# Performance work log

Measured on AMD Instinct MI355X. Metric: run time of the kernel, lower is better.

The kernel has to match this reference:

```python
import jax, jax.numpy as jnp
import numpy as np

B, T = 2, 512
E, NH, HD, V, P, L, KER, BLOCK = 768, 12, 64, 256, 4, 4, 16, 512
SCALE = HD ** -0.5


def _ln(x, g, b, eps=1e-5):
    m = jnp.mean(x, -1, keepdims=True)
    v = jnp.mean((x - m) ** 2, -1, keepdims=True)
    return (x - m) * jax.lax.rsqrt(v + eps) * g + b


def _rope_tables(n):
    inv = 1.0 / (10000.0 ** (jnp.arange(0, HD, 2, dtype=jnp.float32) / HD))
    f = jnp.arange(n, dtype=jnp.float32)[:, None] * inv[None, :]
    return jnp.cos(f), jnp.sin(f)


def _rope(x, cos, sin):
    # rotate over last two dims (positions, HD); split-half RoPE as in source
    h = x.shape[-1] // 2
    x1, x2 = x[..., :h], x[..., h:]
    return jnp.concatenate([x1 * cos - x2 * sin, x1 * sin + x2 * cos], axis=-1)


def _patch_attn(x, qkv_w, S):
    # x: [B,T,E]; sliding-window patch attention, step=1
    Bb, Tt, _ = x.shape
    q, k, v = jnp.split(x @ qkv_w, 3, axis=-1)
    heads = lambda t: t.reshape(Bb, Tt, NH, HD).transpose(0, 2, 1, 3)  # [B,NH,T,HD]
    q, k, v = heads(q), heads(k), heads(v)
    cos, sin = _rope_tables(Tt)
    q = _rope(q, cos, sin)
    k = _rope(k, cos, sin)
    # prefix: full causal attention over first S tokens
    sc = jnp.einsum('bnqh,bnkh->bnqk', q[:, :, :S], k[:, :, :S]) * SCALE
    mask = jnp.tril(jnp.ones((S, S), dtype=bool))
    sc = jnp.where(mask, sc, jnp.float32(-jnp.inf))
    out = jnp.einsum('bnqk,bnkh->bnqh', jax.nn.softmax(sc, axis=-1), v[:, :, :S])
    if Tt > S:
        # query t (t>=S) attends keys [t-S+1, t] (mask_sliding is all-ones for step=1)
        idx = jnp.arange(Tt - S)[:, None] + 1 + jnp.arange(S)[None, :]  # [T-S,S]
        kw = k[:, :, idx]  # [B,NH,T-S,S,HD]
        vw = v[:, :, idx]
        qs = q[:, :, S:]   # [B,NH,T-S,HD]
        sw = jnp.einsum('bnth,bntsh->bnts', qs, kw) * SCALE
        ow = jnp.einsum('bnts,bntsh->bnth', jax.nn.softmax(sw, axis=-1), vw)
        out = jnp.concatenate([out, ow], axis=2)
    return out.transpose(0, 2, 1, 3).reshape(Bb, Tt, NH * HD)


def _sa_block(x, ln0g, ln0b, ln1g, ln1b, qkv_w, proj_w, proj_b, w1, b1, w2, b2):
    # x: [B,T,P,V]; full (unmasked) attention over the P prediction slots
    Bb, Tt, Pp, _ = x.shape
    h = _ln(x, ln0g, ln0b)
    q, k, v = jnp.split(h @ qkv_w, 3, axis=-1)
    heads = lambda t: t.reshape(Bb, Tt, Pp, NH, HD).transpose(0, 1, 3, 2, 4)  # [B,T,NH,P,HD]
    q, k, v = heads(q), heads(k), heads(v)
    cos, sin = _rope_tables(Pp)
    q = _rope(q, cos, sin)
    k = _rope(k, cos, sin)
    sc = jnp.einsum('btnph,btnqh->btnpq', q, k) * SCALE
    o = jnp.einsum('btnpq,btnqh->btnph', jax.nn.softmax(sc, axis=-1), v)
    o = o.transpose(0, 1, 3, 2, 4).reshape(Bb, Tt, Pp, NH * HD)
    x = x + (o @ proj_w + proj_b)
    h2 = _ln(x, ln1g, ln1b)
    ff = jax.nn.gelu(h2 @ w1 + b1, approximate=False) @ w2 + b2
    return x + ff


def _forward(tokens, emb, blk_ln0_g, blk_ln0_b, blk_ln1_g, blk_ln1_b, blk_qkv_w,
             blk_ff_w1, blk_ff_b1, blk_ff_w2, blk_ff_b2, fin_ln_g, fin_ln_b,
             head_w, head_b, sa_ln0_g, sa_ln0_b, sa_ln1_g, sa_ln1_b, sa_qkv_w,
             sa_proj_w, sa_proj_b, sa_ff_w1, sa_ff_b1, sa_ff_w2, sa_ff_b2):
    x0 = emb[tokens]  # [B,T,E]
    x = x0
    for i in range(L):
        S = min(KER * 2 ** i, BLOCK)
        h = _ln(x, blk_ln0_g[i], blk_ln0_b[i])
        x = x + _patch_attn(h, blk_qkv_w[i], S)
        h2 = _ln(x, blk_ln1_g[i], blk_ln1_b[i])
        x = x + (jax.nn.gelu(h2 @ blk_ff_w1[i] + blk_ff_b1[i], approximate=False)
                 @ blk_ff_w2[i] + blk_ff_b2[i])
    x = x0 + x  # Golu: x = token_embedding(x); x = x + blocks(x)
    x = _ln(x, fin_ln_g, fin_ln_b)
    logits = (x @ head_w + head_b).reshape(B, T, P, V)
    logits = _sa_block(logits, sa_ln0_g, sa_ln0_b, sa_ln1_g, sa_ln1_b, sa_qkv_w,
                       sa_proj_w, sa_proj_b, sa_ff_w1, sa_ff_b1, sa_ff_w2, sa_ff_b2)
    return logits[:, :, 0, :]  # [B,T,V] (y is None path)


def setup_inputs() -> dict:
    key = jax.random.key(0)
    ks = jax.random.split(key, 12)
    w = lambda k, sh: jax.random.normal(k, sh, dtype=jnp.float32) * 0.02
    return {
        'tokens': jax.random.randint(ks[0], (B, T), 0, V),
        'emb': w(ks[1], (V, E)),
        'blk_ln0_g': jnp.ones((L, E), jnp.float32),
        'blk_ln0_b': jnp.zeros((L, E), jnp.float32),
        'blk_ln1_g': jnp.ones((L, E), jnp.float32),
        'blk_ln1_b': jnp.zeros((L, E), jnp.float32),
        'blk_qkv_w': w(ks[2], (L, E, 3 * E)),
        'blk_ff_w1': w(ks[3], (L, E, 4 * E)),
        'blk_ff_b1': jnp.zeros((L, 4 * E), jnp.float32),
        'blk_ff_w2': w(ks[4], (L, 4 * E, E)),
        'blk_ff_b2': jnp.zeros((L, E), jnp.float32),
        'fin_ln_g': jnp.ones((E,), jnp.float32),
        'fin_ln_b': jnp.zeros((E,), jnp.float32),
        'head_w': w(ks[5], (E, V * P)),
        'head_b': jnp.zeros((V * P,), jnp.float32),
        'sa_ln0_g': jnp.ones((V,), jnp.float32),
        'sa_ln0_b': jnp.zeros((V,), jnp.float32),
        'sa_ln1_g': jnp.ones((V,), jnp.float32),
        'sa_ln1_b': jnp.zeros((V,), jnp.float32),
        'sa_qkv_w': w(ks[6], (V, 3 * E)),
        'sa_proj_w': w(ks[7], (E, V)),
        'sa_proj_b': jnp.zeros((V,), jnp.float32),
        'sa_ff_w1': w(ks[8], (V, 4 * V)),
        'sa_ff_b1': jnp.zeros((4 * V,), jnp.float32),
        'sa_ff_w2': w(ks[9], (4 * V, V)),
        'sa_ff_b2': jnp.zeros((V,), jnp.float32),
    }


def reference(tokens, emb, blk_ln0_g, blk_ln0_b, blk_ln1_g, blk_ln1_b, blk_qkv_w,
              blk_ff_w1, blk_ff_b1, blk_ff_w2, blk_ff_b2, fin_ln_g, fin_ln_b,
              head_w, head_b, sa_ln0_g, sa_ln0_b, sa_ln1_g, sa_ln1_b, sa_qkv_w,
              sa_proj_w, sa_proj_b, sa_ff_w1, sa_ff_b1, sa_ff_w2, sa_ff_b2):
    return _forward(tokens, emb, blk_ln0_g, blk_ln0_b, blk_ln1_g, blk_ln1_b,
                    blk_qkv_w, blk_ff_w1, blk_ff_b1, blk_ff_w2, blk_ff_b2,
                    fin_ln_g, fin_ln_b, head_w, head_b, sa_ln0_g, sa_ln0_b,
                    sa_ln1_g, sa_ln1_b, sa_qkv_w, sa_proj_w, sa_proj_b,
                    sa_ff_w1, sa_ff_b1, sa_ff_w2, sa_ff_b2)
```

## Files before the change

kernel.cpp:

```cpp
#include <hip/hip_runtime.h>
#include <hip/hip_bf16.h>
#include <cstdint>
#include <cstddef>

#define BB    2
#define TSEQ  512
#define EDIM  768
#define NHEAD 12
#define HDIM  64
#define VDIM  256
#define PDIM  4
#define NROW  (BB*TSEQ)
#define NROW2 (BB*TSEQ*PDIM)

typedef __attribute__((ext_vector_type(8))) short short8;
typedef __attribute__((ext_vector_type(4))) short short4v;
typedef __attribute__((ext_vector_type(4))) float floatx4;

__device__ __forceinline__ float gelu_f(float v){
    return 0.5f * v * (1.0f + erff(v * 0.70710678118654752f));
}
__device__ __forceinline__ float b2f(short s){
    unsigned u = ((unsigned)(unsigned short)s) << 16;
    float f; __builtin_memcpy(&f, &u, 4); return f;
}
__device__ __forceinline__ short f2bs(float v){
    __hip_bfloat16 h = __float2bfloat16(v);
    short s; __builtin_memcpy(&s, &h, 2); return s;
}
__device__ __forceinline__ void gload16(const void* g, void* l){
    __builtin_amdgcn_global_load_lds((const __attribute__((address_space(1))) void*)g,
                                     (__attribute__((address_space(3))) void*)l, 16, 0, 0);
}

#define WAITN(n) asm volatile("s_waitcnt vmcnt(" #n ")" ::: "memory")
#define WAIT_STAGE(rem, full, half)                         \
    do{ if((rem) >= 2)      WAITN(full);                    \
        else if((rem) == 1) WAITN(half);                    \
        else                WAITN(0);                       \
        asm volatile("s_barrier" ::: "memory"); }while(0)

struct WD2 { const float* in; __hip_bfloat16* out; int K; int N; int nt; };
struct WDs { WD2 d[17]; };

__global__ __launch_bounds__(256) void wconv_all(WDs a)
{
    int id = blockIdx.x;
    int i = 0;
    while(i < 16 && id >= a.d[i].nt){ id -= a.d[i].nt; i++; }
    WD2 w = a.d[i];
    const int tx = w.N / 128;
    const int n0 = (id % tx) * 128, k0 = (id / tx) * 128;
    __shared__ short t[128*128];
    {
        const int c4 = (threadIdx.x & 31) * 4;
        const int r0 = threadIdx.x >> 5;
        #pragma unroll
        for(int half = 0; half < 2; half++){
            float4 v[8];
            #pragma unroll
            for(int it = 0; it < 8; it++){
                int r = r0 + it*8 + half*64;
                v[it] = *(const float4*)(w.in + (size_t)(k0 + r) * w.N + n0 + c4);
            }
            #pragma unroll
            for(int it = 0; it < 8; it++){
                int r = r0 + it*8 + half*64;
                int nswz = c4 ^ (((r >> 3) & 15) << 2);
                short4v o;
                o[0] = f2bs(v[it].x); o[1] = f2bs(v[it].y);
                o[2] = f2bs(v[it].z); o[3] = f2bs(v[it].w);
                *(short4v*)&t[r*128 + nswz] = o;
            }
        }
    }
    __syncthreads();
    {
        const int k8 = (threadIdx.x & 15) * 8;
        const int nr = threadIdx.x >> 4;
        const int swz = (k8 >> 3) << 2;
        #pragma unroll
        for(int pass = 0; pass < 8; pass++){
            int n = nr + pass*16;
            int nswz = n ^ swz;
            short8 o;
            #pragma unroll
            for(int j = 0; j < 8; j++) o[j] = t[(k8 + j)*128 + nswz];
            *(short8*)((short*)w.out + (size_t)(n0 + n) * w.K + k0 + k8) = o;
        }
    }
}

template<int ACT, int RESID, int OUTBF16, int ROPESA>
__global__ __launch_bounds__(256) void gemm128(
    const short* __restrict__ A, const short* __restrict__ Bt,
    const float* __restrict__ bias, const float* __restrict__ resid,
    void* __restrict__ Cout, const float* __restrict__ rc, const float* __restrict__ rs,
    int M, int N, int K)
{
    alignas(16) __shared__ short As[4*128*32];
    alignas(16) __shared__ short Bs[4*128*32];
    const int tid  = threadIdx.x;
    const int lane = tid & 63;
    const int wave = tid >> 6;
    const int bm = blockIdx.y * 128, bn = blockIdx.x * 128;
    const int wm = (wave >> 1) * 64, wn = (wave & 1) * 64;
    const int quad = lane >> 4, l16 = lane & 15;

    floatx4 acc[4][4];
    #pragma unroll
    for(int i = 0; i < 4; i++)
        #pragma unroll
        for(int j = 0; j < 4; j++)
            acc[i][j] = floatx4{0.f, 0.f, 0.f, 0.f};

    const int r  = tid >> 2;
    const int c8 = (tid & 3) * 8;
    const int ldsoff = (tid & 192) * 16;

    auto issue = [&](int k0, int cur){
        char* ab = (char*)As + cur*8192 + ldsoff;
        char* bb = (char*)Bs + cur*8192 + ldsoff;
        gload16(A  + (size_t)(bm + r     ) * K + k0 + c8, ab);
        gload16(A  + (size_t)(bm + r + 64) * K + k0 + c8, ab + 4096);
        gload16(Bt + (size_t)(bn + r     ) * K + k0 + c8, bb);
        gload16(Bt + (size_t)(bn + r + 64) * K + k0 + c8, bb + 4096);
    };

    const int niter = K >> 5;
    issue(0, 0); issue(32, 1); issue(64, 2);
    for(int it = 0; it < niter; it++){
        WAIT_STAGE(niter - 1 - it, 8, 4);
        if(it + 3 < niter) issue((it + 3) << 5, (it + 3) & 3);
        const short* Ab = As + (it & 3) * 4096;
        const short* Bb = Bs + (it & 3) * 4096;
        short8 af[4], bfr[4];
        #pragma unroll
        for(int i = 0; i < 4; i++){
            af[i]  = *(const short8*)&Ab[(wm + i*16 + l16)*32 + quad*8];
            bfr[i] = *(const short8*)&Bb[(wn + i*16 + l16)*32 + quad*8];
        }
        #pragma unroll
        for(int i = 0; i < 4; i++)
            #pragma unroll
            for(int j = 0; j < 4; j++)
                acc[i][j] = __builtin_amdgcn_mfma_f32_16x16x32_bf16(af[i], bfr[j], acc[i][j], 0, 0, 0);
    }

    float* Cf = (float*)Cout;
    __hip_bfloat16* Cb = (__hip_bfloat16*)Cout;

    if(ROPESA){
        const int hb = bn + wn;
        const int region = hb / 768;
        #pragma unroll
        for(int i = 0; i < 4; i++){
            #pragma unroll
            for(int rr = 0; rr < 4; rr++){
                int row = bm + wm + i*16 + quad*4 + rr;
                float a0 = acc[i][0][rr], a1 = acc[i][1][rr];
                float a2 = acc[i][2][rr], a3 = acc[i][3][rr];
                size_t rowb = (size_t)row * N + hb;
                if(region == 2){
                    Cb[rowb + l16]      = __float2bfloat16(a0);
                    Cb[rowb + 16 + l16] = __float2bfloat16(a1);
                    Cb[rowb + 32 + l16] = __float2bfloat16(a2);
                    Cb[rowb + 48 + l16] = __float2bfloat16(a3);
                }else{
                    int p = row & 3;
                    float c0 = rc[p*32 + l16],      s0 = rs[p*32 + l16];
                    float c1 = rc[p*32 + 16 + l16], s1 = rs[p*32 + 16 + l16];
                    Cb[rowb + l16]      = __float2bfloat16(a0*c0 - a2*s0);
                    Cb[rowb + 16 + l16] = __float2bfloat16(a1*c1 - a3*s1);
                    Cb[rowb + 32 + l16] = __float2bfloat16(a0*s0 + a2*c0);
                    Cb[rowb + 48 + l16] = __float2bfloat16(a1*s1 + a3*c1);
                }
            }
        }
        return;
    }

    #pragma unroll
    for(int i = 0; i < 4; i++){
        int row0 = bm + wm + i*16 + quad*4;
        #pragma unroll
        for(int j = 0; j < 4; j++){
            int col = bn + wn + j*16 + l16;
            float bv = bias ? bias[col] : 0.f;
            #pragma unroll
            for(int rr = 0; rr < 4; rr++){
                float v = acc[i][j][rr] + bv;
                if(ACT) v = gelu_f(v);
                if(RESID) v += resid[(size_t)(row0 + rr) * N + col];
                if(OUTBF16) Cb[(size_t)(row0 + rr) * N + col] = __float2bfloat16(v);
                else        Cf[(size_t)(row0 + rr) * N + col] = v;
            }
        }
    }
}

template<int EPI>
__global__ __launch_bounds__(256) void gemm64x128(
    const short* __restrict__ A, const short* __restrict__ Bt,
    const float* __restrict__ bias, __hip_bfloat16* __restrict__ Cout,
    __hip_bfloat16* __restrict__ qrb, __hip_bfloat16* __restrict__ krb,
    __hip_bfloat16* __restrict__ vvb,
    const float* __restrict__ rc, const float* __restrict__ rs,
    int M, int N, int K)
{
    alignas(16) __shared__ short As[4*64*32];
    alignas(16) __shared__ short Bs[4*128*32];
    const int tid  = threadIdx.x;
    const int lane = tid & 63;
    const int wave = tid >> 6;
    const int bm = blockIdx.y * 64, bn = blockIdx.x * 128;
    const int wm = (wave >> 1) * 32, wn = (wave & 1) * 64;
    const int quad = lane >> 4, l16 = lane & 15;

    floatx4 acc[2][4];
    #pragma unroll
    for(int i = 0; i < 2; i++)
        #pragma unroll
        for(int j = 0; j < 4; j++)
            acc[i][j] = floatx4{0.f, 0.f, 0.f, 0.f};

    const int r  = tid >> 2;
    const int c8 = (tid & 3) * 8;
    const int ldsoff = (tid & 192) * 16;

    auto issue = [&](int k0, int cur){
        char* ab = (char*)As + cur*4096 + ldsoff;
        char* bb = (char*)Bs + cur*8192 + ldsoff;
        gload16(A  + (size_t)(bm + r     ) * K + k0 + c8, ab);
        gload16(Bt + (size_t)(bn + r     ) * K + k0 + c8, bb);
        gload16(Bt + (size_t)(bn + r + 64) * K + k0 + c8, bb + 4096);
    };

    const int niter = K >> 5;
    issue(0, 0); issue(32, 1); issue(64, 2);
    for(int it = 0; it < niter; it++){
        WAIT_STAGE(niter - 1 - it, 6, 3);
        if(it + 3 < niter) issue((it + 3) << 5, (it + 3) & 3);
        const short* Ab = As + (it & 3) * 2048;
        const short* Bb = Bs + (it & 3) * 4096;
        short8 af[2], bfr[4];
        #pragma unroll
        for(int i = 0; i < 2; i++)
            af[i]  = *(const short8*)&Ab[(wm + i*16 + l16)*32 + quad*8];
        #pragma unroll
        for(int j = 0; j < 4; j++)
            bfr[j] = *(const short8*)&Bb[(wn + j*16 + l16)*32 + quad*8];
        #pragma unroll
        for(int i = 0; i < 2; i++)
            #pragma unroll
            for(int j = 0; j < 4; j++)
                acc[i][j] = __builtin_amdgcn_mfma_f32_16x16x32_bf16(af[i], bfr[j], acc[i][j], 0, 0, 0);
    }

    if(EPI == 2){
        const int hb = bn + wn;
        const int region = hb / 768;
        const int h = (hb % 768) >> 6;
        #pragma unroll
        for(int i = 0; i < 2; i++){
            #pragma unroll
            for(int rr = 0; rr < 4; rr++){
                int row = bm + wm + i*16 + quad*4 + rr;
                int t = row & (TSEQ-1), b = row >> 9;
                float a0 = acc[i][0][rr], a1 = acc[i][1][rr];
                float a2 = acc[i][2][rr], a3 = acc[i][3][rr];
                size_t dbase = ((size_t)(b*NHEAD + h)*TSEQ + t)*HDIM;
                if(region == 2){
                    vvb[dbase + l16]      = __float2bfloat16(a0);
                    vvb[dbase + 16 + l16] = __float2bfloat16(a1);
                    vvb[dbase + 32 + l16] = __float2bfloat16(a2);
                    vvb[dbase + 48 + l16] = __float2bfloat16(a3);
                }else{
                    float c0 = rc[t*32 + l16],      s0 = rs[t*32 + l16];
                    float c1 = rc[t*32 + 16 + l16], s1 = rs[t*32 + 16 + l16];
                    __hip_bfloat16* dst = (region == 0) ? qrb : krb;
                    dst[dbase + l16]      = __float2bfloat16(a0*c0 - a2*s0);
                    dst[dbase + 16 + l16] = __float2bfloat16(a1*c1 - a3*s1);
                    dst[dbase + 32 + l16] = __float2bfloat16(a0*s0 + a2*c0);
                    dst[dbase + 48 + l16] = __float2bfloat16(a1*s1 + a3*c1);
                }
            }
        }
        return;
    }

    #pragma unroll
    for(int i = 0; i < 2; i++){
        int row0 = bm + wm + i*16 + quad*4;
        #pragma unroll
        for(int j = 0; j < 4; j++){
            int col = bn + wn + j*16 + l16;
            float bv = bias ? bias[col] : 0.f;
            #pragma unroll
            for(int rr = 0; rr < 4; rr++){
                float v = acc[i][j][rr] + bv;
                if(EPI == 1) v = gelu_f(v);
                Cout[(size_t)(row0 + rr) * N + col] = __float2bfloat16(v);
            }
        }
    }
}

template<int RESID, int OUTC>
__global__ __launch_bounds__(256) void gemm64t(
    const short* __restrict__ A, const short* __restrict__ Bt,
    const float* __restrict__ bias, const float* __restrict__ resid,
    float* __restrict__ Cf, float* __restrict__ outp, int M, int N, int K)
{
    alignas(16) __shared__ short As[4*64*32];
    alignas(16) __shared__ short Bs[4*64*32];
    const int tid  = threadIdx.x;
    const int lane = tid & 63;
    const int wave = tid >> 6;
    const int bm = blockIdx.y * 64, bn = blockIdx.x * 64;
    const int wm = (wave >> 1) * 32, wn = (wave & 1) * 32;
    const int quad = lane >> 4, l16 = lane & 15;

    floatx4 acc[2][2];
    #pragma unroll
    for(int i = 0; i < 2; i++)
        #pragma unroll
        for(int j = 0; j < 2; j++)
            acc[i][j] = floatx4{0.f, 0.f, 0.f, 0.f};

    const int r  = tid >> 2;
    const int c8 = (tid & 3) * 8;
    const int ldsoff = (tid & 192) * 16;

    auto issue = [&](int k0, int cur){
        char* ab = (char*)As + cur*4096 + ldsoff;
        char* bb = (char*)Bs + cur*4096 + ldsoff;
        gload16(A  + (size_t)(bm + r) * K + k0 + c8, ab);
        gload16(Bt + (size_t)(bn + r) * K + k0 + c8, bb);
    };

    const int niter = K >> 5;
    issue(0, 0); issue(32, 1); issue(64, 2);
    for(int it = 0; it < niter; it++){
        WAIT_STAGE(niter - 1 - it, 4, 2);
        if(it + 3 < niter) issue((it + 3) << 5, (it + 3) & 3);
        const short* Ab = As + (it & 3) * 2048;
        const short* Bb = Bs + (it & 3) * 2048;
        short8 af[2], bfr[2];
        #pragma unroll
        for(int i = 0; i < 2; i++){
            af[i]  = *(const short8*)&Ab[(wm + i*16 + l16)*32 + quad*8];
            bfr[i] = *(const short8*)&Bb[(wn + i*16 + l16)*32 + quad*8];
        }
        #pragma unroll
        for(int i = 0; i < 2; i++)
            #pragma unroll
            for(int j = 0; j < 2; j++)
                acc[i][j] = __builtin_amdgcn_mfma_f32_16x16x32_bf16(af[i], bfr[j], acc[i][j], 0, 0, 0);
    }

    #pragma unroll
    for(int i = 0; i < 2; i++){
        int row0 = bm + wm + i*16 + quad*4;
        #pragma unroll
        for(int j = 0; j < 2; j++){
            int col = bn + wn + j*16 + l16;
            float bv = bias ? bias[col] : 0.f;
            #pragma unroll
            for(int rr = 0; rr < 4; rr++){
                int row = row0 + rr;
                float v = acc[i][j][rr] + bv;
                if(RESID) v += resid[(size_t)row * N + col];
                Cf[(size_t)row * N + col] = v;
                if(OUTC && (row & 3) == 0)
                    outp[(size_t)(row >> 2) * N + col] = v;
            }
        }
    }
}

template<int D>
__global__ __launch_bounds__(256) void ln_wave(
    const float* __restrict__ in, const float* __restrict__ in2,
    const float* __restrict__ g, const float* __restrict__ bta,
    __hip_bfloat16* __restrict__ out)
{
    constexpr int NC = D / 256;
    const int row  = blockIdx.x * 4 + (threadIdx.x >> 6);
    const int lane = threadIdx.x & 63;
    const float* xr = in + (size_t)row * D;
    float4 v[NC];
    float sum = 0.f, sq = 0.f;
    #pragma unroll
    for(int j = 0; j < NC; j++){
        int d0 = (lane + 64*j) * 4;
        v[j] = *(const float4*)(xr + d0);
        if(in2){
            float4 u = *(const float4*)(in2 + (size_t)row * D + d0);
            v[j].x += u.x; v[j].y += u.y; v[j].z += u.z; v[j].w += u.w;
        }
        sum += v[j].x + v[j].y + v[j].z + v[j].w;
        sq  += v[j].x*v[j].x + v[j].y*v[j].y + v[j].z*v[j].z + v[j].w*v[j].w;
    }
    #pragma unroll
    for(int off = 32; off > 0; off >>= 1){
        sum += __shfl_xor(sum, off, 64);
        sq  += __shfl_xor(sq,  off, 64);
    }
    const float m    = sum / D;
    const float rstd = rsqrtf(fmaxf(sq / D - m*m, 0.f) + 1e-5f);
    #pragma unroll
    for(int j = 0; j < NC; j++){
        int d0 = (lane + 64*j) * 4;
        float4 gg = *(const float4*)(g + d0);
        float4 bb = *(const float4*)(bta + d0);
        short4v o;
        o[0] = f2bs((v[j].x - m) * rstd * gg.x + bb.x);
        o[1] = f2bs((v[j].y - m) * rstd * gg.y + bb.y);
        o[2] = f2bs((v[j].z - m) * rstd * gg.z + bb.z);
        o[3] = f2bs((v[j].w - m) * rstd * gg.w + bb.w);
        *(short4v*)((short*)out + (size_t)row * D + d0) = o;
    }
}

__global__ __launch_bounds__(192) void embed_kernel(
    const int* __restrict__ tokens, const float* __restrict__ emb,
    float* __restrict__ x0, float* __restrict__ x)
{
    const int row = blockIdx.x;
    const int tok = tokens[row];
    const float4* src = (const float4*)(emb + (size_t)tok * EDIM);
    float4* d0 = (float4*)(x0 + (size_t)row * EDIM);
    float4* d1 = (float4*)(x  + (size_t)row * EDIM);
    for(int i = threadIdx.x; i < EDIM/4; i += blockDim.x){
        float4 v = src[i]; d0[i] = v; d1[i] = v;
    }
}

__global__ __launch_bounds__(256) void rope_kernel(float* __restrict__ rc, float* __restrict__ rs)
{
    int i = blockIdx.x * 256 + threadIdx.x;
    int pos = i >> 5, d = i & 31;
    float inv = powf(10000.0f, -(float)(2*d) / 64.0f);
    float f = (float)pos * inv;
    rc[i] = cosf(f);
    rs[i] = sinf(f);
}

template<int S>
__global__ __launch_bounds__(256) void patch_attn16(
    const __hip_bfloat16* __restrict__ qr, const __hip_bfloat16* __restrict__ kr,
    const __hip_bfloat16* __restrict__ vv, float* __restrict__ x)
{
    constexpr int W = S + 15;
    alignas(16) __shared__ short Ks[W*64];
    alignas(16) __shared__ short Vs[W*64];
    __shared__ float qlds[16*64];
    __shared__ float pb[16*128];

    const int t0 = blockIdx.x * 16;
    const int h = blockIdx.y, b = blockIdx.z;
    const int tid = threadIdx.x;
    const int wv = tid >> 6, lane = tid & 63;
    const size_t headbase = ((size_t)(b*NHEAD + h)) * TSEQ;

    const int c = tid & 7;
    for(int r = tid >> 3; r < W; r += 32){
        int g = t0 - S + 1 + r;
        int gc = g < 0 ? 0 : g;
        int sc = (c ^ (r & 7)) * 8;
        *(short8*)&Ks[r*64 + sc] = *(const short8*)((const short*)kr + (headbase + gc)*64 + c*8);
        *(short8*)&Vs[r*64 + sc] = *(const short8*)((const short*)vv + (headbase + gc)*64 + c*8);
    }
    for(int i = tid; i < 16*64; i += 256)
        qlds[i] = __bfloat162float(qr[(headbase + t0 + (i >> 6))*64 + (i & 63)]);
    __syncthreads();

    #pragma unroll
    for(int qq = 0; qq < 4; qq++){
        const int ql = wv*4 + qq;
        const int t  = t0 + ql;
        const int r0 = (S >= 64) ? (ql + lane) : ((lane < S) ? (ql + lane) : 0);
        const int r1 = ql + lane + 64;
        float a0 = 0.f, a1 = 0.f;
        #pragma unroll
        for(int ch = 0; ch < 8; ch++){
            float4 qa = *(const float4*)&qlds[ql*64 + ch*8];
            float4 qb = *(const float4*)&qlds[ql*64 + ch*8 + 4];
            short8 k0 = *(const short8*)&Ks[r0*64 + ((ch ^ (r0 & 7))*8)];
            a0 += qa.x*b2f(k0[0]) + qa.y*b2f(k0[1]) + qa.z*b2f(k0[2]) + qa.w*b2f(k0[3])
                + qb.x*b2f(k0[4]) + qb.y*b2f(k0[5]) + qb.z*b2f(k0[6]) + qb.w*b2f(k0[7]);
            if(S == 128){
                short8 k1 = *(const short8*)&Ks[r1*64 + ((ch ^ (r1 & 7))*8)];
                a1 += qa.x*b2f(k1[0]) + qa.y*b2f(k1[1]) + qa.z*b2f(k1[2]) + qa.w*b2f(k1[3])
                    + qb.x*b2f(k1[4]) + qb.y*b2f(k1[5]) + qb.z*b2f(k1[6]) + qb.w*b2f(k1[7]);
            }
        }
        const int key0 = t - S + 1 + lane;
        const bool v0 = (lane < S) && (key0 >= 0);
        const bool v1 = (S == 128) && (key0 + 64 >= 0);
        float s0 = v0 ? a0 * 0.125f : -1e30f;
        float s1 = v1 ? a1 * 0.125f : -1e30f;
        float mx = fmaxf(s0, s1);
        #pragma unroll
        for(int off = 32; off > 0; off >>= 1) mx = fmaxf(mx, __shfl_xor(mx, off, 64));
        float p0 = v0 ? expf(s0 - mx) : 0.f;
        float p1 = v1 ? expf(s1 - mx) : 0.f;
        float sm = p0 + p1;
        #pragma unroll
        for(int off = 32; off > 0; off >>= 1) sm += __shfl_xor(sm, off, 64);
        const float inv = 1.f / sm;
        pb[ql*128 + lane] = p0 * inv;
        if(S == 128) pb[ql*128 + lane + 64] = p1 * inv;
    }

    const int d = lane;
    const int coff = d >> 3, dlo = d & 7;
    #pragma unroll
    for(int qq = 0; qq < 4; qq++){
        const int ql = wv*4 + qq;
        float o = 0.f;
        #pragma unroll 8
        for(int j = 0; j < S; j++){
            int r = ql + j;
            float p = pb[ql*128 + j];
            o += p * b2f(Vs[r*64 + ((coff ^ (r & 7))*8) + dlo]);
        }
        x[((size_t)(b*TSEQ) + t0 + ql) * EDIM + h*HDIM + d] += o;
    }
}

__global__ __launch_bounds__(256) void sa_attn(
    const __hip_bfloat16* __restrict__ qkv2, __hip_bfloat16* __restrict__ o)
{
    const int t = blockIdx.x, h = blockIdx.y, b = blockIdx.z;
    const int p = threadIdx.x >> 6, lane = threadIdx.x & 63;
    const int row0 = (b*TSEQ + t) * PDIM;
    const short* base = (const short*)qkv2 + (size_t)row0 * (3*EDIM);
    const int d = lane;
    float q = b2f(base[(size_t)p*(3*EDIM) + h*HDIM + d]);
    float sc[4];
    #pragma unroll
    for(int j = 0; j < 4; j++){
        float kj = b2f(base[(size_t)j*(3*EDIM) + EDIM + h*HDIM + d]);
        float v = q * kj;
        #pragma unroll
        for(int off = 32; off > 0; off >>= 1) v += __shfl_xor(v, off, 64);
        sc[j] = v * 0.125f;
    }
    float m = fmaxf(fmaxf(sc[0], sc[1]), fmaxf(sc[2], sc[3]));
    float e0 = expf(sc[0]-m), e1 = expf(sc[1]-m), e2 = expf(sc[2]-m), e3 = expf(sc[3]-m);
    float idn = 1.f / (e0 + e1 + e2 + e3);
    float ov = (e0 * b2f(base[0*(3*EDIM) + 2*EDIM + h*HDIM + d])
              + e1 * b2f(base[1*(3*EDIM) + 2*EDIM + h*HDIM + d])
              + e2 * b2f(base[2*(3*EDIM) + 2*EDIM + h*HDIM + d])
              + e3 * b2f(base[3*(3*EDIM) + 2*EDIM + h*HDIM + d])) * idn;
    o[(size_t)(row0 + p) * EDIM + h*HDIM + d] = __float2bfloat16(ov);
}

extern "C" void kernel_launch(void* const* d_in, const int* in_sizes, int n_in,
                              void* d_out, int out_size, void* d_ws, size_t ws_size,
                              hipStream_t stream)
{
    const int*   tokens    = (const int*)  d_in[0];
    const float* emb       = (const float*)d_in[1];
    const float* bl0g      = (const float*)d_in[2];
    const float* bl0b      = (const float*)d_in[3];
    const float* bl1g      = (const float*)d_in[4];
    const float* bl1b      = (const float*)d_in[5];
    const float* qkv_w     = (const float*)d_in[6];
    const float* ff_w1     = (const float*)d_in[7];
    const float* ff_b1     = (const float*)d_in[8];
    const float* ff_w2     = (const float*)d_in[9];
    const float* ff_b2     = (const float*)d_in[10];
    const float* fin_g     = (const float*)d_in[11];
    const float* fin_b     = (const float*)d_in[12];
    const float* head_w    = (const float*)d_in[13];
    const float* head_b    = (const float*)d_in[14];
    const float* sa_ln0_g  = (const float*)d_in[15];
    const float* sa_ln0_b  = (const float*)d_in[16];
    const float* sa_ln1_g  = (const float*)d_in[17];
    const float* sa_ln1_b  = (const float*)d_in[18];
    const float* sa_qkv_w  = (const float*)d_in[19];
    const float* sa_proj_w = (const float*)d_in[20];
    const float* sa_proj_b = (const float*)d_in[21];
    const float* sa_ff_w1  = (const float*)d_in[22];
    const float* sa_ff_b1  = (const float*)d_in[23];
    const float* sa_ff_w2  = (const float*)d_in[24];
    const float* sa_ff_b2  = (const float*)d_in[25];
    float* out = (float*)d_out;

    char* p = (char*)d_ws;
    auto alloc = [&](size_t bytes){ char* q = p; p += (bytes + 255) & ~(size_t)255; return q; };

    float* logits = (float*)alloc((size_t)NROW2*VDIM*4);
    float* ropec  = (float*)alloc(512*32*4);
    float* ropes  = (float*)alloc(512*32*4);
    __hip_bfloat16* wqkvT[4]; for(int i=0;i<4;i++) wqkvT[i] = (__hip_bfloat16*)alloc((size_t)768*2304*2);
    __hip_bfloat16* wff1T[4]; for(int i=0;i<4;i++) wff1T[i] = (__hip_bfloat16*)alloc((size_t)768*3072*2);
    __hip_bfloat16* wff2T[4]; for(int i=0;i<4;i++) wff2T[i] = (__hip_bfloat16*)alloc((size_t)3072*768*2);
    __hip_bfloat16* wheadT   = (__hip_bfloat16*)alloc((size_t)768*1024*2);
    __hip_bfloat16* wsaqkvT  = (__hip_bfloat16*)alloc((size_t)256*2304*2);
    __hip_bfloat16* wsaprojT = (__hip_bfloat16*)alloc((size_t)768*256*2);
    __hip_bfloat16* wsaff1T  = (__hip_bfloat16*)alloc((size_t)256*1024*2);
    __hip_bfloat16* wsaff2T  = (__hip_bfloat16*)alloc((size_t)1024*256*2);
    char* U = p;
    float* x0           = (float*)(U);
    float* x            = (float*)(U + 3145728);
    __hip_bfloat16* h   = (__hip_bfloat16*)(U + 6291456);
    __hip_bfloat16* ff1 = (__hip_bfloat16*)(U + 7864320);
    __hip_bfloat16* qrb = (__hip_bfloat16*)(U + 14155776);
    __hip_bfloat16* krb = (__hip_bfloat16*)(U + 15728640);
    __hip_bfloat16* vvb = (__hip_bfloat16*)(U + 17301504);
    __hip_bfloat16* h2    = (__hip_bfloat16*)(U);
    __hip_bfloat16* qkv2  = (__hip_bfloat16*)(U + 2097152);
    __hip_bfloat16* sa_o  = (__hip_bfloat16*)(U + 20971520);
    __hip_bfloat16* sa_f1 = (__hip_bfloat16*)(U + 27262976);

    embed_kernel<<<NROW, 192, 0, stream>>>(tokens, emb, x0, x);
    rope_kernel<<<64, 256, 0, stream>>>(ropec, ropes);
    {
        WDs wds; int tot = 0, n = 0;
        auto add = [&](const float* in, __hip_bfloat16* o2, int K, int N){
            wds.d[n++] = WD2{in, o2, K, N, (N/128)*(K/128)};
            tot += (N/128)*(K/128);
        };
        for(int i=0;i<4;i++){
            add(qkv_w + (size_t)i*768*2304, wqkvT[i], 768, 2304);
            add(ff_w1 + (size_t)i*768*3072, wff1T[i], 768, 3072);
            add(ff_w2 + (size_t)i*3072*768, wff2T[i], 3072, 768);
        }
        add(head_w,    wheadT,   768, 1024);
        add(sa_qkv_w,  wsaqkvT,  256, 2304);
        add(sa_proj_w, wsaprojT, 768, 256);
        add(sa_ff_w1,  wsaff1T,  256, 1024);
        add(sa_ff_w2,  wsaff2T, 1024, 256);
        wconv_all<<<tot, 256, 0, stream>>>(wds);
    }

    for(int i = 0; i < 4; i++){
        ln_wave<EDIM><<<NROW/4, 256, 0, stream>>>(x, nullptr, bl0g + i*EDIM, bl0b + i*EDIM, h);
        gemm64x128<2><<<dim3(18, 16), 256, 0, stream>>>(
            (const short*)h, (const short*)wqkvT[i], nullptr, nullptr,
            qrb, krb, vvb, ropec, ropes, NROW, 3*EDIM, EDIM);
        dim3 agrid(TSEQ/16, NHEAD, BB);
        if(i == 0)      patch_attn16<16><<<agrid, 256, 0, stream>>>(qrb, krb, vvb, x);
        else if(i == 1) patch_attn16<32><<<agrid, 256, 0, stream>>>(qrb, krb, vvb, x);
        else if(i == 2) patch_attn16<64><<<agrid, 256, 0, stream>>>(qrb, krb, vvb, x);
        else            patch_attn16<128><<<agrid, 256, 0, stream>>>(qrb, krb, vvb, x);
        ln_wave<EDIM><<<NROW/4, 256, 0, stream>>>(x, nullptr, bl1g + i*EDIM, bl1b + i*EDIM, h);
        gemm64x128<1><<<dim3(24, 16), 256, 0, stream>>>(
            (const short*)h, (const short*)wff1T[i], ff_b1 + (size_t)i*4*EDIM, ff1,
            nullptr, nullptr, nullptr, nullptr, nullptr, NROW, 4*EDIM, EDIM);
        gemm64t<1,0><<<dim3(12, 16), 256, 0, stream>>>(
            (const short*)ff1, (const short*)wff2T[i], ff_b2 + (size_t)i*EDIM, x, x, nullptr,
            NROW, EDIM, 4*EDIM);
    }

    ln_wave<EDIM><<<NROW/4, 256, 0, stream>>>(x, x0, fin_g, fin_b, h);
    gemm64t<0,0><<<dim3(16, 16), 256, 0, stream>>>(
        (const short*)h, (const short*)wheadT, head_b, nullptr, logits, nullptr,
        NROW, PDIM*VDIM, EDIM);

    ln_wave<VDIM><<<NROW2/4, 256, 0, stream>>>(logits, nullptr, sa_ln0_g, sa_ln0_b, h2);
    gemm128<0,0,1,1><<<dim3(18, 32), 256, 0, stream>>>(
        (const short*)h2, (const short*)wsaqkvT, nullptr, nullptr, qkv2,
        ropec, ropes, NROW2, 3*EDIM, VDIM);
    sa_attn<<<dim3(TSEQ, NHEAD, BB), 256, 0, stream>>>(qkv2, sa_o);
    gemm64t<1,0><<<dim3(4, 64), 256, 0, stream>>>(
        (const short*)sa_o, (const short*)wsaprojT, sa_proj_b, logits, logits, nullptr,
        NROW2, VDIM, EDIM);
    ln_wave<VDIM><<<NROW2/4, 256, 0, stream>>>(logits, nullptr, sa_ln1_g, sa_ln1_b, h2);
    gemm128<1,0,1,0><<<dim3(8, 32), 256, 0, stream>>>(
        (const short*)h2, (const short*)wsaff1T, sa_ff_b1, nullptr, sa_f1,
        nullptr, nullptr, NROW2, 4*VDIM, VDIM);
    gemm64t<1,1><<<dim3(4, 64), 256, 0, stream>>>(
        (const short*)sa_f1, (const short*)wsaff2T, sa_ff_b2, logits, logits, out,
        NROW2, VDIM, 4*VDIM);
}
```

Measured before the change: 698.8 us.

## Move QKV and FF1 GEMMs to 128x128 tiles, fuse embed/rope, loop heads in sa_attn

Drops the 64x128 GEMM kernel and runs the transformer-block QKV and FF1 GEMMs with the 128x128 gemm128 kernel, which gains a RoPE/head-scatter epilogue mode. Embedding and RoPE table generation are merged into one launch. sa_attn now loops over all 12 heads within a block instead of launching one block per head. Larger tiles give more operand reuse per block, but the grids shrink to 144 and 192 blocks, which may underfill the GPU's compute units. The sa_attn change does more serial work per block and launches 12x fewer blocks.

```diff
diff --git a/kernel.cpp b/kernel.cpp
--- a/kernel.cpp
+++ b/kernel.cpp
@@ -96,6 +96,8 @@
     const short* __restrict__ A, const short* __restrict__ Bt,
     const float* __restrict__ bias, const float* __restrict__ resid,
     void* __restrict__ Cout, const float* __restrict__ rc, const float* __restrict__ rs,
+    __hip_bfloat16* __restrict__ qrb, __hip_bfloat16* __restrict__ krb,
+    __hip_bfloat16* __restrict__ vvb,
     int M, int N, int K)
 {
     alignas(16) __shared__ short As[4*128*32];
@@ -150,7 +152,7 @@
     float* Cf = (float*)Cout;
     __hip_bfloat16* Cb = (__hip_bfloat16*)Cout;
 
-    if(ROPESA){
+    if(ROPESA == 1){
         const int hb = bn + wn;
         const int region = hb / 768;
         #pragma unroll
@@ -180,89 +182,12 @@
         return;
     }
 
-    #pragma unroll
-    for(int i = 0; i < 4; i++){
-        int row0 = bm + wm + i*16 + quad*4;
-        #pragma unroll
-        for(int j = 0; j < 4; j++){
-            int col = bn + wn + j*16 + l16;
-            float bv = bias ? bias[col] : 0.f;
-            #pragma unroll
-            for(int rr = 0; rr < 4; rr++){
-                float v = acc[i][j][rr] + bv;
-                if(ACT) v = gelu_f(v);
-                if(RESID) v += resid[(size_t)(row0 + rr) * N + col];
-                if(OUTBF16) Cb[(size_t)(row0 + rr) * N + col] = __float2bfloat16(v);
-                else        Cf[(size_t)(row0 + rr) * N + col] = v;
-            }
-        }
-    }
-}
-
-template<int EPI>
-__global__ __launch_bounds__(256) void gemm64x128(
-    const short* __restrict__ A, const short* __restrict__ Bt,
-    const float* __restrict__ bias, __hip_bfloat16* __restrict__ Cout,
-    __hip_bfloat16* __restrict__ qrb, __hip_bfloat16* __restrict__ krb,
-    __hip_bfloat16* __restrict__ vvb,
-    const float* __restrict__ rc, const float* __restrict__ rs,
-    int M, int N, int K)
-{
-    alignas(16) __shared__ short As[4*64*32];
-    alignas(16) __shared__ short Bs[4*128*32];
-    const int tid  = threadIdx.x;
-    const int lane = tid & 63;
-    const int wave = tid >> 6;
-    const int bm = blockIdx.y * 64, bn = blockIdx.x * 128;
-    const int wm = (wave >> 1) * 32, wn = (wave & 1) * 64;
-    const int quad = lane >> 4, l16 = lane & 15;
-
-    floatx4 acc[2][4];
-    #pragma unroll
-    for(int i = 0; i < 2; i++)
-        #pragma unroll
-        for(int j = 0; j < 4; j++)
-            acc[i][j] = floatx4{0.f, 0.f, 0.f, 0.f};
-
-    const int r  = tid >> 2;
-    const int c8 = (tid & 3) * 8;
-    const int ldsoff = (tid & 192) * 16;
-
-    auto issue = [&](int k0, int cur){
-        char* ab = (char*)As + cur*4096 + ldsoff;
-        char* bb = (char*)Bs + cur*8192 + ldsoff;
-        gload16(A  + (size_t)(bm + r     ) * K + k0 + c8, ab);
-        gload16(Bt + (size_t)(bn + r     ) * K + k0 + c8, bb);
-        gload16(Bt + (size_t)(bn + r + 64) * K + k0 + c8, bb + 4096);
-    };
-
-    const int niter = K >> 5;
-    issue(0, 0); issue(32, 1); issue(64, 2);
-    for(int it = 0; it < niter; it++){
-        WAIT_STAGE(niter - 1 - it, 6, 3);
-        if(it + 3 < niter) issue((it + 3) << 5, (it + 3) & 3);
-        const short* Ab = As + (it & 3) * 2048;
-        const short* Bb = Bs + (it & 3) * 4096;
-        short8 af[2], bfr[4];
-        #pragma unroll
-        for(int i = 0; i < 2; i++)
-            af[i]  = *(const short8*)&Ab[(wm + i*16 + l16)*32 + quad*8];
-        #pragma unroll
-        for(int j = 0; j < 4; j++)
-            bfr[j] = *(const short8*)&Bb[(wn + j*16 + l16)*32 + quad*8];
-        #pragma unroll
-        for(int i = 0; i < 2; i++)
-            #pragma unroll
-            for(int j = 0; j < 4; j++)
-                acc[i][j] = __builtin_amdgcn_mfma_f32_16x16x32_bf16(af[i], bfr[j], acc[i][j], 0, 0, 0);
-    }
-
-    if(EPI == 2){
+    if(ROPESA == 2){
         const int hb = bn + wn;
         const int region = hb / 768;
         const int h = (hb % 768) >> 6;
         #pragma unroll
-        for(int i = 0; i < 2; i++){
+        for(int i = 0; i < 4; i++){
             #pragma unroll
             for(int rr = 0; rr < 4; rr++){
                 int row = bm + wm + i*16 + quad*4 + rr;
@@ -290,7 +215,7 @@
     }
 
     #pragma unroll
-    for(int i = 0; i < 2; i++){
+    for(int i = 0; i < 4; i++){
         int row0 = bm + wm + i*16 + quad*4;
         #pragma unroll
         for(int j = 0; j < 4; j++){
@@ -299,8 +224,10 @@
             #pragma unroll
             for(int rr = 0; rr < 4; rr++){
                 float v = acc[i][j][rr] + bv;
-                if(EPI == 1) v = gelu_f(v);
-                Cout[(size_t)(row0 + rr) * N + col] = __float2bfloat16(v);
+                if(ACT) v = gelu_f(v);
+                if(RESID) v += resid[(size_t)(row0 + rr) * N + col];
+                if(OUTBF16) Cb[(size_t)(row0 + rr) * N + col] = __float2bfloat16(v);
+                else        Cf[(size_t)(row0 + rr) * N + col] = v;
             }
         }
     }
@@ -423,23 +350,23 @@
     }
 }
 
-__global__ __launch_bounds__(192) void embed_kernel(
+__global__ __launch_bounds__(256) void embed_rope(
     const int* __restrict__ tokens, const float* __restrict__ emb,
-    float* __restrict__ x0, float* __restrict__ x)
-{
-    const int row = blockIdx.x;
-    const int tok = tokens[row];
-    const float4* src = (const float4*)(emb + (size_t)tok * EDIM);
-    float4* d0 = (float4*)(x0 + (size_t)row * EDIM);
-    float4* d1 = (float4*)(x  + (size_t)row * EDIM);
-    for(int i = threadIdx.x; i < EDIM/4; i += blockDim.x){
-        float4 v = src[i]; d0[i] = v; d1[i] = v;
-    }
-}
-
-__global__ __launch_bounds__(256) void rope_kernel(float* __restrict__ rc, float* __restrict__ rs)
-{
-    int i = blockIdx.x * 256 + threadIdx.x;
+    float* __restrict__ x0, float* __restrict__ x,
+    float* __restrict__ rc, float* __restrict__ rs)
+{
+    const int blk = blockIdx.x;
+    if(blk < NROW){
+        const int tok = tokens[blk];
+        const float4* src = (const float4*)(emb + (size_t)tok * EDIM);
+        float4* d0 = (float4*)(x0 + (size_t)blk * EDIM);
+        float4* d1 = (float4*)(x  + (size_t)blk * EDIM);
+        if(threadIdx.x < EDIM/4){
+            float4 v = src[threadIdx.x]; d0[threadIdx.x] = v; d1[threadIdx.x] = v;
+        }
+        return;
+    }
+    int i = (blk - NROW) * 256 + threadIdx.x;
     int pos = i >> 5, d = i & 31;
     float inv = powf(10000.0f, -(float)(2*d) / 64.0f);
     float f = (float)pos * inv;
@@ -533,29 +460,31 @@
 __global__ __launch_bounds__(256) void sa_attn(
     const __hip_bfloat16* __restrict__ qkv2, __hip_bfloat16* __restrict__ o)
 {
-    const int t = blockIdx.x, h = blockIdx.y, b = blockIdx.z;
+    const int t = blockIdx.x, b = blockIdx.z;
     const int p = threadIdx.x >> 6, lane = threadIdx.x & 63;
     const int row0 = (b*TSEQ + t) * PDIM;
     const short* base = (const short*)qkv2 + (size_t)row0 * (3*EDIM);
     const int d = lane;
-    float q = b2f(base[(size_t)p*(3*EDIM) + h*HDIM + d]);
-    float sc[4];
-    #pragma unroll
-    for(int j = 0; j < 4; j++){
-        float kj = b2f(base[(size_t)j*(3*EDIM) + EDIM + h*HDIM + d]);
-        float v = q * kj;
-        #pragma unroll
-        for(int off = 32; off > 0; off >>= 1) v += __shfl_xor(v, off, 64);
-        sc[j] = v * 0.125f;
-    }
-    float m = fmaxf(fmaxf(sc[0], sc[1]), fmaxf(sc[2], sc[3]));
-    float e0 = expf(sc[0]-m), e1 = expf(sc[1]-m), e2 = expf(sc[2]-m), e3 = expf(sc[3]-m);
-    float idn = 1.f / (e0 + e1 + e2 + e3);
-    float ov = (e0 * b2f(base[0*(3*EDIM) + 2*EDIM + h*HDIM + d])
-              + e1 * b2f(base[1*(3*EDIM) + 2*EDIM + h*HDIM + d])
-              + e2 * b2f(base[2*(3*EDIM) + 2*EDIM + h*HDIM + d])
-              + e3 * b2f(base[3*(3*EDIM) + 2*EDIM + h*HDIM + d])) * idn;
-    o[(size_t)(row0 + p) * EDIM + h*HDIM + d] = __float2bfloat16(ov);
+    for(int h = 0; h < NHEAD; h++){
+        float q = b2f(base[(size_t)p*(3*EDIM) + h*HDIM + d]);
+        float sc[4];
+        #pragma unroll
+        for(int j = 0; j < 4; j++){
+            float kj = b2f(base[(size_t)j*(3*EDIM) + EDIM + h*HDIM + d]);
+            float v = q * kj;
+            #pragma unroll
+            for(int off = 32; off > 0; off >>= 1) v += __shfl_xor(v, off, 64);
+            sc[j] = v * 0.125f;
+        }
+        float m = fmaxf(fmaxf(sc[0], sc[1]), fmaxf(sc[2], sc[3]));
+        float e0 = expf(sc[0]-m), e1 = expf(sc[1]-m), e2 = expf(sc[2]-m), e3 = expf(sc[3]-m);
+        float idn = 1.f / (e0 + e1 + e2 + e3);
+        float ov = (e0 * b2f(base[0*(3*EDIM) + 2*EDIM + h*HDIM + d])
+                  + e1 * b2f(base[1*(3*EDIM) + 2*EDIM + h*HDIM + d])
+                  + e2 * b2f(base[2*(3*EDIM) + 2*EDIM + h*HDIM + d])
+                  + e3 * b2f(base[3*(3*EDIM) + 2*EDIM + h*HDIM + d])) * idn;
+        o[(size_t)(row0 + p) * EDIM + h*HDIM + d] = __float2bfloat16(ov);
+    }
 }
 
 extern "C" void kernel_launch(void* const* d_in, const int* in_sizes, int n_in,
@@ -617,8 +546,7 @@
     __hip_bfloat16* sa_o  = (__hip_bfloat16*)(U + 20971520);
     __hip_bfloat16* sa_f1 = (__hip_bfloat16*)(U + 27262976);
 
-    embed_kernel<<<NROW, 192, 0, stream>>>(tokens, emb, x0, x);
-    rope_kernel<<<64, 256, 0, stream>>>(ropec, ropes);
+    embed_rope<<<NROW + 64, 256, 0, stream>>>(tokens, emb, x0, x, ropec, ropes);
     {
         WDs wds; int tot = 0, n = 0;
         auto add = [&](const float* in, __hip_bfloat16* o2, int K, int N){
@@ -640,17 +568,17 @@
 
     for(int i = 0; i < 4; i++){
         ln_wave<EDIM><<<NROW/4, 256, 0, stream>>>(x, nullptr, bl0g + i*EDIM, bl0b + i*EDIM, h);
-        gemm64x128<2><<<dim3(18, 16), 256, 0, stream>>>(
-            (const short*)h, (const short*)wqkvT[i], nullptr, nullptr,
-            qrb, krb, vvb, ropec, ropes, NROW, 3*EDIM, EDIM);
+        gemm128<0,0,1,2><<<dim3(18, 8), 256, 0, stream>>>(
+            (const short*)h, (const short*)wqkvT[i], nullptr, nullptr, nullptr,
+            ropec, ropes, qrb, krb, vvb, NROW, 3*EDIM, EDIM);
         dim3 agrid(TSEQ/16, NHEAD, BB);
         if(i == 0)      patch_attn16<16><<<agrid, 256, 0, stream>>>(qrb, krb, vvb, x);
         else if(i == 1) patch_attn16<32><<<agrid, 256, 0, stream>>>(qrb, krb, vvb, x);
         else if(i == 2) patch_attn16<64><<<agrid, 256, 0, stream>>>(qrb, krb, vvb, x);
         else            patch_attn16<128><<<agrid, 256, 0, stream>>>(qrb, krb, vvb, x);
         ln_wave<EDIM><<<NROW/4, 256, 0, stream>>>(x, nullptr, bl1g + i*EDIM, bl1b + i*EDIM, h);
-        gemm64x128<1><<<dim3(24, 16), 256, 0, stream>>>(
-            (const short*)h, (const short*)wff1T[i], ff_b1 + (size_t)i*4*EDIM, ff1,
+        gemm128<1,0,1,0><<<dim3(24, 8), 256, 0, stream>>>(
+            (const short*)h, (const short*)wff1T[i], ff_b1 + (size_t)i*4*EDIM, nullptr, ff1,
             nullptr, nullptr, nullptr, nullptr, nullptr, NROW, 4*EDIM, EDIM);
         gemm64t<1,0><<<dim3(12, 16), 256, 0, stream>>>(
             (const short*)ff1, (const short*)wff2T[i], ff_b2 + (size_t)i*EDIM, x, x, nullptr,
@@ -665,15 +593,15 @@
     ln_wave<VDIM><<<NROW2/4, 256, 0, stream>>>(logits, nullptr, sa_ln0_g, sa_ln0_b, h2);
     gemm128<0,0,1,1><<<dim3(18, 32), 256, 0, stream>>>(
         (const short*)h2, (const short*)wsaqkvT, nullptr, nullptr, qkv2,
-        ropec, ropes, NROW2, 3*EDIM, VDIM);
-    sa_attn<<<dim3(TSEQ, NHEAD, BB), 256, 0, stream>>>(qkv2, sa_o);
+        ropec, ropes, nullptr, nullptr, nullptr, NROW2, 3*EDIM, VDIM);
+    sa_attn<<<dim3(TSEQ, 1, BB), 256, 0, stream>>>(qkv2, sa_o);
     gemm64t<1,0><<<dim3(4, 64), 256, 0, stream>>>(
         (const short*)sa_o, (const short*)wsaprojT, sa_proj_b, logits, logits, nullptr,
         NROW2, VDIM, EDIM);
     ln_wave<VDIM><<<NROW2/4, 256, 0, stream>>>(logits, nullptr, sa_ln1_g, sa_ln1_b, h2);
     gemm128<1,0,1,0><<<dim3(8, 32), 256, 0, stream>>>(
         (const short*)h2, (const short*)wsaff1T, sa_ff_b1, nullptr, sa_f1,
-        nullptr, nullptr, NROW2, 4*VDIM, VDIM);
+        nullptr, nullptr, nullptr, nullptr, nullptr, NROW2, 4*VDIM, VDIM);
     gemm64t<1,1><<<dim3(4, 64), 256, 0, stream>>>(
         (const short*)sa_f1, (const short*)wsaff2T, sa_ff_b2, logits, logits, out,
         NROW2, VDIM, 4*VDIM);
```

Measured after the change: 752.1 us. 7.6% more time.
